# Optimization experiments

Measured on AMD Instinct MI355X. Metric: run time of the kernel, lower is better.

## Reference

```python
import jax, jax.numpy as jnp
import numpy as np

B, N_ELEC, N_NUC, D_EMB, D_MSG = 512, 32, 8, 128, 128


def idx_perm(n):
    # ordered pairs (i, j), i != j, shaped [n, n-1]
    i = np.repeat(np.arange(n), n - 1).reshape(n, n - 1)
    j = np.array([[k for k in range(n) if k != ii] for ii in range(n)])
    return jnp.asarray(i), jnp.asarray(j)


def pairwise_diffs(a, b):
    # a: [..., n, 3], b: [..., m, 3] -> [..., n, m, 4] (dx, dy, dz, |d|^2)
    d = a[..., :, None, :] - b[..., None, :, :]
    return jnp.concatenate([d, jnp.sum(d * d, axis=-1, keepdims=True)], axis=-1)


def mlp(x, w1, b1, w2, b2):
    return jax.nn.silu(x @ w1 + b1) @ w2 + b2


def setup_inputs() -> dict:
    key = jax.random.key(0)
    ks = jax.random.split(key, 10)
    sc = 0.1
    return {
        'rs': jax.random.normal(ks[0], (B, N_ELEC, 3), jnp.float32),
        'coords': jax.random.normal(ks[1], (N_NUC, 3), jnp.float32),
        'messages_el': jax.random.normal(ks[2], (B, N_ELEC, N_ELEC - 1, D_MSG), jnp.float32),
        'messages_nuc': jax.random.normal(ks[3], (B, N_ELEC, N_NUC, D_MSG), jnp.float32),
        'emb': jax.random.normal(ks[4], (B, N_ELEC, D_EMB), jnp.float32),
        'w1_el': jax.random.normal(ks[5], (D_EMB + D_MSG, 256), jnp.float32) * sc,
        'b1_el': jnp.zeros((256,), jnp.float32),
        'w2_el': jax.random.normal(ks[6], (256, 1), jnp.float32) * sc,
        'b2_el': jnp.zeros((1,), jnp.float32),
        'w1_nuc': jax.random.normal(ks[7], (D_EMB + D_MSG, 256), jnp.float32) * sc,
        'b1_nuc': jnp.zeros((256,), jnp.float32),
        'w2_nuc': jax.random.normal(ks[8], (256, 1), jnp.float32) * sc,
        'b2_nuc': jnp.zeros((1,), jnp.float32),
        'nuc_charges': jnp.array([6.0, 1.0, 1.0, 1.0, 1.0, 1.0, 1.0, 1.0], jnp.float32),
    }


def reference(rs, coords, messages_el, messages_nuc, emb,
              w1_el, b1_el, w2_el, b2_el,
              w1_nuc, b1_nuc, w2_nuc, b2_nuc, nuc_charges):
    n_elec, n_nuc = rs.shape[-2], coords.shape[0]
    emb_p = emb[:, :, None]  # [B, n_elec, 1, D_emb]
    # gather-concat features per pair
    f_el = jnp.concatenate(
        [jnp.broadcast_to(emb_p, (B, n_elec, n_elec - 1, D_EMB)), messages_el], axis=-1)
    f_nuc = jnp.concatenate(
        [jnp.broadcast_to(emb_p, (B, n_elec, n_nuc, D_EMB)), messages_nuc], axis=-1)
    i, j = idx_perm(n_elec)
    diffs_nuc = pairwise_diffs(rs, coords)  # [B, n_elec, n_nuc, 4]
    diffs_ee = pairwise_diffs(-rs, -rs)[:, i, j]  # [B, n_elec, n_elec-1, 4]
    diffs = jnp.concatenate([diffs_ee, diffs_nuc], axis=-2)
    f = jnp.concatenate(
        [mlp(f_el, w1_el, b1_el, w2_el, b2_el),
         mlp(f_nuc, w1_nuc, b1_nuc, w2_nuc, b2_nuc)], axis=-2)  # [B, n_elec, P, 1]
    ps = f * diffs[..., :3] / (1.0 + diffs[..., 3:] ** 1.5)
    ps = ps.sum(axis=-2)  # [B, n_elec, 3]
    # deeperwin decay
    decay = jnp.tanh(diffs_nuc[..., -1] / (0.5 / nuc_charges) ** 2).prod(axis=-1)
    return np.exp(-3.5).astype(np.float32) * decay[..., None] * ps
```

## Files before the change

kernel.cpp:

```cpp
#include <hip/hip_runtime.h>
#include <hip/hip_bf16.h>

#define OUT_SCALE 0.030197383422318501f

typedef __attribute__((ext_vector_type(8))) short bf16x8;
typedef __attribute__((ext_vector_type(4))) float f32x4;

#define EL_BLOCKS 2048
#define NUC_BLOCKS 1024

__device__ __forceinline__ unsigned pk2(float a, float b) {
  __hip_bfloat162 h = __float22bfloat162_rn(make_float2(a, b));
  unsigned u;
  __builtin_memcpy(&u, &h, 4);
  return u;
}

__device__ __forceinline__ float silu_f(float h) {
  return h * __builtin_amdgcn_rcpf(1.0f + __expf(-h));
}

__global__ void prep_w1(const float* __restrict__ w1a,
                        const float* __restrict__ w1b,
                        unsigned short* __restrict__ wp) {
  int gid = blockIdx.x * 256 + threadIdx.x;
  const float* w1 = (gid < 8192) ? w1a : w1b;
  int rem = gid & 8191;
  int kk = rem >> 10;
  int kg = (rem >> 8) & 3;
  int col = rem & 255;
  const float* src = w1 + (kk * 32 + kg * 8) * 256 + col;
  uint4 v;
  v.x = pk2(src[0 * 256], src[1 * 256]);
  v.y = pk2(src[2 * 256], src[3 * 256]);
  v.z = pk2(src[4 * 256], src[5 * 256]);
  v.w = pk2(src[6 * 256], src[7 * 256]);
  *(uint4*)(wp + (size_t)gid * 8) = v;
}

__global__ __launch_bounds__(512, 4) void bf_main_kernel(
    const float* __restrict__ rs, const float* __restrict__ msg_el,
    const float* __restrict__ msg_nuc, const float* __restrict__ emb,
    const unsigned short* __restrict__ wpk,
    const float* __restrict__ b1_el, const float* __restrict__ w2_el,
    const float* __restrict__ b2_el,
    const float* __restrict__ b1_nuc, const float* __restrict__ w2_nuc,
    const float* __restrict__ b2_nuc,
    const float* __restrict__ coords, const float* __restrict__ chg,
    float* __restrict__ out) {
  __shared__ __align__(16) unsigned short s_emb[16 * 128];
  __shared__ __align__(16) unsigned short s_msg[2 * 64 * 128];
  __shared__ __align__(16) float s_embc[16 * 256];
  __shared__ float s_fp[8][256];
  __shared__ float s_ps[16][4];
  __shared__ float s_decay[16];

  const int tid = threadIdx.x;
  const int bid = blockIdx.x;
  const int lane = tid & 63;
  const int wv = tid >> 6;
  const int cIdx = lane & 15, kg = lane >> 4;

  if (bid < EL_BLOCKS) {
    const int gp0 = bid * 8;
    const float* msg = msg_el;

    if (tid < 32) ((float*)s_ps)[tid] = 0.0f;

    {
      int p = tid >> 4, ch = tid & 15;
      if (tid < 128) {
        const float* src = emb + (gp0 + p) * 128 + ch * 8;
        float4 v0 = *(const float4*)src;
        float4 v1 = *(const float4*)(src + 4);
        uint4 pk;
        pk.x = pk2(v0.x, v0.y); pk.y = pk2(v0.z, v0.w);
        pk.z = pk2(v1.x, v1.y); pk.w = pk2(v1.z, v1.w);
        *(uint4*)(s_emb + p * 128 + (ch ^ (p & 15)) * 8) = pk;
      } else if (tid < 256) {
        uint4 z = {0u, 0u, 0u, 0u};
        *(uint4*)(s_emb + p * 128 + (ch ^ (p & 15)) * 8) = z;
      }
    }

    bf16x8 Bf[4][2];
    float b1v[2][4], w2v[2][4];
    const int col = wv * 32 + cIdx;
#pragma unroll
    for (int nt = 0; nt < 2; ++nt) {
#pragma unroll
      for (int reg = 0; reg < 4; ++reg) {
        int h = wv * 32 + nt * 16 + kg * 4 + reg;
        b1v[nt][reg] = b1_el[h];
        w2v[nt][reg] = w2_el[h];
      }
#pragma unroll
      for (int kk = 0; kk < 4; ++kk)
        Bf[kk][nt] = *(const bf16x8*)(
            wpk + (size_t)((kk * 4 + kg) * 256 + col + nt * 16) * 8);
    }

    float4 la[2], lb[2];
    bool lv[2];
#pragma unroll
    for (int u = 0; u < 2; ++u) {
      int id = u * 512 + tid;
      int lr = id >> 4, ch = id & 15;
      int p = lr >> 5, j = lr & 31;
      lv[u] = j < 31;
      const float* src =
          msg + (size_t)((gp0 + p) * 31 + (lv[u] ? j : 30)) * 128 + ch * 8;
      la[u] = *(const float4*)src;
      lb[u] = *(const float4*)(src + 4);
    }

    __syncthreads();

    {
      f32x4 aE0 = {b1v[0][0], b1v[0][1], b1v[0][2], b1v[0][3]};
      f32x4 aE1 = {b1v[1][0], b1v[1][1], b1v[1][2], b1v[1][3]};
#pragma unroll
      for (int kk = 0; kk < 4; ++kk) {
        bf16x8 a = *(const bf16x8*)(
            s_emb + cIdx * 128 + ((kk * 4 + kg) ^ (cIdx & 15)) * 8);
        aE0 = __builtin_amdgcn_mfma_f32_16x16x32_bf16(Bf[kk][0], a, aE0, 0, 0, 0);
        aE1 = __builtin_amdgcn_mfma_f32_16x16x32_bf16(Bf[kk][1], a, aE1, 0, 0, 0);
      }
      if (cIdx < 8) {
        *(f32x4*)(s_embc + cIdx * 256 + wv * 32 + kg * 4) = aE0;
        *(f32x4*)(s_embc + cIdx * 256 + wv * 32 + 16 + kg * 4) = aE1;
      }
    }

#pragma unroll
    for (int nt = 0; nt < 2; ++nt)
#pragma unroll
      for (int kk = 0; kk < 4; ++kk)
        Bf[kk][nt] = *(const bf16x8*)(
            wpk + (size_t)(((kk + 4) * 4 + kg) * 256 + col + nt * 16) * 8);

#pragma unroll
    for (int u = 0; u < 2; ++u) {
      int id = u * 512 + tid;
      int lr = id >> 4, ch = id & 15;
      uint4 pk;
      pk.x = lv[u] ? pk2(la[u].x, la[u].y) : 0u;
      pk.y = lv[u] ? pk2(la[u].z, la[u].w) : 0u;
      pk.z = lv[u] ? pk2(lb[u].x, lb[u].y) : 0u;
      pk.w = lv[u] ? pk2(lb[u].z, lb[u].w) : 0u;
      *(uint4*)(s_msg + lr * 128 + ((ch ^ (lr & 15)) * 8)) = pk;
    }

    __syncthreads();

#pragma unroll 1
    for (int c = 0; c < 4; ++c) {
      if (c < 3) {
#pragma unroll
        for (int u = 0; u < 2; ++u) {
          int id = u * 512 + tid;
          int lr = id >> 4, ch = id & 15;
          int row = (c + 1) * 64 + lr;
          int p = row >> 5, j = row & 31;
          lv[u] = j < 31;
          const float* src =
              msg + (size_t)((gp0 + p) * 31 + (lv[u] ? j : 30)) * 128 + ch * 8;
          la[u] = *(const float4*)src;
          lb[u] = *(const float4*)(src + 4);
        }
      }
      const unsigned short* mb = s_msg + (c & 1) * 8192;
#pragma unroll
      for (int tt = 0; tt < 4; ++tt) {
        int t = c * 4 + tt;
        int p = t >> 1;
        int r = t * 16 + cIdx;
        f32x4 acc0 = *(const f32x4*)(s_embc + p * 256 + wv * 32 + kg * 4);
        f32x4 acc1 = *(const f32x4*)(s_embc + p * 256 + wv * 32 + 16 + kg * 4);
        const unsigned short* mp = mb + (r & 63) * 128;
#pragma unroll
        for (int kk = 0; kk < 4; ++kk) {
          bf16x8 a = *(const bf16x8*)(mp + ((kk * 4 + kg) ^ (r & 15)) * 8);
          acc0 = __builtin_amdgcn_mfma_f32_16x16x32_bf16(Bf[kk][0], a, acc0, 0, 0, 0);
          acc1 = __builtin_amdgcn_mfma_f32_16x16x32_bf16(Bf[kk][1], a, acc1, 0, 0, 0);
        }
        float p0 = 0.0f, p1 = 0.0f;
#pragma unroll
        for (int reg = 0; reg < 4; ++reg) {
          p0 += silu_f(acc0[reg]) * w2v[0][reg];
          p1 += silu_f(acc1[reg]) * w2v[1][reg];
        }
        float v = p0 + p1;
        v += __shfl_xor(v, 16);
        v += __shfl_xor(v, 32);
        if (kg == 0) s_fp[wv][t * 16 + cIdx] = v;
      }
      if (c < 3) {
#pragma unroll
        for (int u = 0; u < 2; ++u) {
          int id = u * 512 + tid;
          int lr = id >> 4, ch = id & 15;
          uint4 pk;
          pk.x = lv[u] ? pk2(la[u].x, la[u].y) : 0u;
          pk.y = lv[u] ? pk2(la[u].z, la[u].w) : 0u;
          pk.z = lv[u] ? pk2(lb[u].x, lb[u].y) : 0u;
          pk.w = lv[u] ? pk2(lb[u].z, lb[u].w) : 0u;
          *(uint4*)(s_msg + ((c + 1) & 1) * 8192 + lr * 128 +
                    ((ch ^ (lr & 15)) * 8)) = pk;
        }
      }
      __syncthreads();
    }

    if (tid < 248) {
      int p = tid / 31, jj = tid - p * 31;
      int gp = gp0 + p, b = gp >> 5, i = gp & 31;
      int jidx = jj + (jj >= i ? 1 : 0);
      const float* rsb = rs + b * 96;
      float dx = rsb[jidx * 3 + 0] - rsb[i * 3 + 0];
      float dy = rsb[jidx * 3 + 1] - rsb[i * 3 + 1];
      float dz = rsb[jidx * 3 + 2] - rsb[i * 3 + 2];
      float tq = dx * dx + dy * dy + dz * dz;
      int row = p * 32 + jj;
      float f = b2_el[0];
#pragma unroll
      for (int w = 0; w < 8; ++w) f += s_fp[w][row];
      float g = f * __builtin_amdgcn_rcpf(1.0f + tq * sqrtf(tq));
      atomicAdd(&s_ps[p][0], g * dx);
      atomicAdd(&s_ps[p][1], g * dy);
      atomicAdd(&s_ps[p][2], g * dz);
    }
    if (tid < 8) {
      int gp = gp0 + tid, b = gp >> 5, i = gp & 31;
      float x = rs[(b * 32 + i) * 3 + 0];
      float y = rs[(b * 32 + i) * 3 + 1];
      float z = rs[(b * 32 + i) * 3 + 2];
      float dcy = 1.0f;
#pragma unroll
      for (int n = 0; n < 8; ++n) {
        float dx = x - coords[n * 3 + 0];
        float dy = y - coords[n * 3 + 1];
        float dz = z - coords[n * 3 + 2];
        float tq = dx * dx + dy * dy + dz * dz;
        float zc = chg[n];
        dcy *= tanhf(4.0f * tq * zc * zc);
      }
      s_decay[tid] = dcy;
    }
    __syncthreads();
    if (tid < 24) {
      int p = tid / 3, c = tid - p * 3;
      int gp = gp0 + p;
      atomicAdd(&out[gp * 3 + c], OUT_SCALE * s_decay[p] * s_ps[p][c]);
    }
  } else {
    const int nbid = bid - EL_BLOCKS;
    const int gp0 = nbid * 16;
    const float* msg = msg_nuc;
    const unsigned short* wp = wpk + 8192 * 8;

    if (tid < 64) ((float*)s_ps)[tid] = 0.0f;

    if (tid < 256) {
      int p = tid >> 4, ch = tid & 15;
      const float* src = emb + (gp0 + p) * 128 + ch * 8;
      float4 v0 = *(const float4*)src;
      float4 v1 = *(const float4*)(src + 4);
      uint4 pk;
      pk.x = pk2(v0.x, v0.y); pk.y = pk2(v0.z, v0.w);
      pk.z = pk2(v1.x, v1.y); pk.w = pk2(v1.z, v1.w);
      *(uint4*)(s_emb + p * 128 + (ch ^ (p & 15)) * 8) = pk;
    }

    bf16x8 Bf[4][2];
    float b1v[2][4], w2v[2][4];
    const int col = wv * 32 + cIdx;
#pragma unroll
    for (int nt = 0; nt < 2; ++nt) {
#pragma unroll
      for (int reg = 0; reg < 4; ++reg) {
        int h = wv * 32 + nt * 16 + kg * 4 + reg;
        b1v[nt][reg] = b1_nuc[h];
        w2v[nt][reg] = w2_nuc[h];
      }
#pragma unroll
      for (int kk = 0; kk < 4; ++kk)
        Bf[kk][nt] = *(const bf16x8*)(
            wp + (size_t)((kk * 4 + kg) * 256 + col + nt * 16) * 8);
    }

    float4 la[2], lb[2];
#pragma unroll
    for (int u = 0; u < 2; ++u) {
      int id = u * 512 + tid;
      int lr = id >> 4, ch = id & 15;
      const float* src = msg + (size_t)(gp0 * 8 + lr) * 128 + ch * 8;
      la[u] = *(const float4*)src;
      lb[u] = *(const float4*)(src + 4);
    }

    __syncthreads();

    {
      f32x4 aE0 = {b1v[0][0], b1v[0][1], b1v[0][2], b1v[0][3]};
      f32x4 aE1 = {b1v[1][0], b1v[1][1], b1v[1][2], b1v[1][3]};
#pragma unroll
      for (int kk = 0; kk < 4; ++kk) {
        bf16x8 a = *(const bf16x8*)(
            s_emb + cIdx * 128 + ((kk * 4 + kg) ^ (cIdx & 15)) * 8);
        aE0 = __builtin_amdgcn_mfma_f32_16x16x32_bf16(Bf[kk][0], a, aE0, 0, 0, 0);
        aE1 = __builtin_amdgcn_mfma_f32_16x16x32_bf16(Bf[kk][1], a, aE1, 0, 0, 0);
      }
      *(f32x4*)(s_embc + cIdx * 256 + wv * 32 + kg * 4) = aE0;
      *(f32x4*)(s_embc + cIdx * 256 + wv * 32 + 16 + kg * 4) = aE1;
    }

#pragma unroll
    for (int nt = 0; nt < 2; ++nt)
#pragma unroll
      for (int kk = 0; kk < 4; ++kk)
        Bf[kk][nt] = *(const bf16x8*)(
            wp + (size_t)(((kk + 4) * 4 + kg) * 256 + col + nt * 16) * 8);

#pragma unroll
    for (int u = 0; u < 2; ++u) {
      int id = u * 512 + tid;
      int lr = id >> 4, ch = id & 15;
      uint4 pk;
      pk.x = pk2(la[u].x, la[u].y);
      pk.y = pk2(la[u].z, la[u].w);
      pk.z = pk2(lb[u].x, lb[u].y);
      pk.w = pk2(lb[u].z, lb[u].w);
      *(uint4*)(s_msg + lr * 128 + ((ch ^ (lr & 15)) * 8)) = pk;
    }

    __syncthreads();

#pragma unroll 1
    for (int c = 0; c < 2; ++c) {
      if (c < 1) {
#pragma unroll
        for (int u = 0; u < 2; ++u) {
          int id = u * 512 + tid;
          int lr = id >> 4, ch = id & 15;
          const float* src =
              msg + (size_t)(gp0 * 8 + 64 + lr) * 128 + ch * 8;
          la[u] = *(const float4*)src;
          lb[u] = *(const float4*)(src + 4);
        }
      }
      const unsigned short* mb = s_msg + (c & 1) * 8192;
#pragma unroll
      for (int tt = 0; tt < 4; ++tt) {
        int t = c * 4 + tt;
        int r = t * 16 + cIdx;
        int p = r >> 3;
        f32x4 acc0 = *(const f32x4*)(s_embc + p * 256 + wv * 32 + kg * 4);
        f32x4 acc1 = *(const f32x4*)(s_embc + p * 256 + wv * 32 + 16 + kg * 4);
        const unsigned short* mp = mb + (r & 63) * 128;
#pragma unroll
        for (int kk = 0; kk < 4; ++kk) {
          bf16x8 a = *(const bf16x8*)(mp + ((kk * 4 + kg) ^ (r & 15)) * 8);
          acc0 = __builtin_amdgcn_mfma_f32_16x16x32_bf16(Bf[kk][0], a, acc0, 0, 0, 0);
          acc1 = __builtin_amdgcn_mfma_f32_16x16x32_bf16(Bf[kk][1], a, acc1, 0, 0, 0);
        }
        float p0 = 0.0f, p1 = 0.0f;
#pragma unroll
        for (int reg = 0; reg < 4; ++reg) {
          p0 += silu_f(acc0[reg]) * w2v[0][reg];
          p1 += silu_f(acc1[reg]) * w2v[1][reg];
        }
        float v = p0 + p1;
        v += __shfl_xor(v, 16);
        v += __shfl_xor(v, 32);
        if (kg == 0) s_fp[wv][t * 16 + cIdx] = v;
      }
      if (c < 1) {
#pragma unroll
        for (int u = 0; u < 2; ++u) {
          int id = u * 512 + tid;
          int lr = id >> 4, ch = id & 15;
          uint4 pk;
          pk.x = pk2(la[u].x, la[u].y);
          pk.y = pk2(la[u].z, la[u].w);
          pk.z = pk2(lb[u].x, lb[u].y);
          pk.w = pk2(lb[u].z, lb[u].w);
          *(uint4*)(s_msg + 8192 + lr * 128 + ((ch ^ (lr & 15)) * 8)) = pk;
        }
      }
      __syncthreads();
    }

    if (tid < 128) {
      int p = tid >> 3, n = tid & 7;
      int gp = gp0 + p, b = gp >> 5, i = gp & 31;
      float dx = rs[(b * 32 + i) * 3 + 0] - coords[n * 3 + 0];
      float dy = rs[(b * 32 + i) * 3 + 1] - coords[n * 3 + 1];
      float dz = rs[(b * 32 + i) * 3 + 2] - coords[n * 3 + 2];
      float tq = dx * dx + dy * dy + dz * dz;
      float f = b2_nuc[0];
#pragma unroll
      for (int w = 0; w < 8; ++w) f += s_fp[w][tid];
      float g = f * __builtin_amdgcn_rcpf(1.0f + tq * sqrtf(tq));
      atomicAdd(&s_ps[p][0], g * dx);
      atomicAdd(&s_ps[p][1], g * dy);
      atomicAdd(&s_ps[p][2], g * dz);
    }
    if (tid < 16) {
      int gp = gp0 + tid, b = gp >> 5, i = gp & 31;
      float x = rs[(b * 32 + i) * 3 + 0];
      float y = rs[(b * 32 + i) * 3 + 1];
      float z = rs[(b * 32 + i) * 3 + 2];
      float dcy = 1.0f;
#pragma unroll
      for (int n = 0; n < 8; ++n) {
        float dx = x - coords[n * 3 + 0];
        float dy = y - coords[n * 3 + 1];
        float dz = z - coords[n * 3 + 2];
        float tq = dx * dx + dy * dy + dz * dz;
        float zc = chg[n];
        dcy *= tanhf(4.0f * tq * zc * zc);
      }
      s_decay[tid] = dcy;
    }
    __syncthreads();
    if (tid < 48) {
      int p = tid / 3, c = tid - p * 3;
      int gp = gp0 + p;
      atomicAdd(&out[gp * 3 + c], OUT_SCALE * s_decay[p] * s_ps[p][c]);
    }
  }
}

extern "C" void kernel_launch(void* const* d_in, const int* in_sizes, int n_in,
                              void* d_out, int out_size, void* d_ws, size_t ws_size,
                              hipStream_t stream) {
  const float* rs       = (const float*)d_in[0];
  const float* coords   = (const float*)d_in[1];
  const float* msg_el   = (const float*)d_in[2];
  const float* msg_nuc  = (const float*)d_in[3];
  const float* emb      = (const float*)d_in[4];
  const float* w1_el    = (const float*)d_in[5];
  const float* b1_el    = (const float*)d_in[6];
  const float* w2_el    = (const float*)d_in[7];
  const float* b2_el    = (const float*)d_in[8];
  const float* w1_nuc   = (const float*)d_in[9];
  const float* b1_nuc   = (const float*)d_in[10];
  const float* w2_nuc   = (const float*)d_in[11];
  const float* b2_nuc   = (const float*)d_in[12];
  const float* chg      = (const float*)d_in[13];
  float* out = (float*)d_out;

  unsigned short* wpk = (unsigned short*)d_ws;

  hipMemsetAsync(out, 0, (size_t)out_size * sizeof(float), stream);
  prep_w1<<<64, 256, 0, stream>>>(w1_el, w1_nuc, wpk);
  bf_main_kernel<<<EL_BLOCKS + NUC_BLOCKS, 512, 0, stream>>>(
      rs, msg_el, msg_nuc, emb, wpk, b1_el, w2_el, b2_el, b1_nuc, w2_nuc,
      b2_nuc, coords, chg, out);
}
```

Measured before the change: 120.8 us.

## Process sixteen electrons per electron-pair block and drop padding zeroing

Electron-pair blocks now handle 16 electrons each instead of 8, halving the electron block count. The per-block embedding projection fills the full 16-row MFMA tile instead of zero-padding half of it, and the weight fragment loads are amortized over twice the work. Padded pair rows are loaded from a duplicate row rather than zeroed, since their outputs are unused. In exchange, each block does a longer serial chunk loop and uses more shared memory, and the grid has fewer blocks for latency hiding.

Result: faster. 114.8 us, median of 2 (-4.9%).

```diff
diff --git a/kernel.cpp b/kernel.cpp
--- a/kernel.cpp
+++ b/kernel.cpp
@@ -6,7 +6,7 @@
 typedef __attribute__((ext_vector_type(8))) short bf16x8;
 typedef __attribute__((ext_vector_type(4))) float f32x4;
 
-#define EL_BLOCKS 2048
+#define EL_BLOCKS 1024
 #define NUC_BLOCKS 1024
 
 __device__ __forceinline__ unsigned pk2(float a, float b) {
@@ -51,7 +51,7 @@
   __shared__ __align__(16) unsigned short s_emb[16 * 128];
   __shared__ __align__(16) unsigned short s_msg[2 * 64 * 128];
   __shared__ __align__(16) float s_embc[16 * 256];
-  __shared__ float s_fp[8][256];
+  __shared__ float s_fp[8][512];
   __shared__ float s_ps[16][4];
   __shared__ float s_decay[16];
 
@@ -62,25 +62,20 @@
   const int cIdx = lane & 15, kg = lane >> 4;
 
   if (bid < EL_BLOCKS) {
-    const int gp0 = bid * 8;
+    const int gp0 = bid * 16;
     const float* msg = msg_el;
 
-    if (tid < 32) ((float*)s_ps)[tid] = 0.0f;
-
-    {
+    if (tid < 64) ((float*)s_ps)[tid] = 0.0f;
+
+    if (tid < 256) {
       int p = tid >> 4, ch = tid & 15;
-      if (tid < 128) {
-        const float* src = emb + (gp0 + p) * 128 + ch * 8;
-        float4 v0 = *(const float4*)src;
-        float4 v1 = *(const float4*)(src + 4);
-        uint4 pk;
-        pk.x = pk2(v0.x, v0.y); pk.y = pk2(v0.z, v0.w);
-        pk.z = pk2(v1.x, v1.y); pk.w = pk2(v1.z, v1.w);
-        *(uint4*)(s_emb + p * 128 + (ch ^ (p & 15)) * 8) = pk;
-      } else if (tid < 256) {
-        uint4 z = {0u, 0u, 0u, 0u};
-        *(uint4*)(s_emb + p * 128 + (ch ^ (p & 15)) * 8) = z;
-      }
+      const float* src = emb + (gp0 + p) * 128 + ch * 8;
+      float4 v0 = *(const float4*)src;
+      float4 v1 = *(const float4*)(src + 4);
+      uint4 pk;
+      pk.x = pk2(v0.x, v0.y); pk.y = pk2(v0.z, v0.w);
+      pk.z = pk2(v1.x, v1.y); pk.w = pk2(v1.z, v1.w);
+      *(uint4*)(s_emb + p * 128 + (ch ^ p) * 8) = pk;
     }
 
     bf16x8 Bf[4][2];
@@ -101,17 +96,15 @@
     }
 
     float4 la[2], lb[2];
-    bool lv[2];
 #pragma unroll
     for (int u = 0; u < 2; ++u) {
       int id = u * 512 + tid;
-      int lr = id >> 4, ch = id & 15;
-      int p = lr >> 5, j = lr & 31;
-      lv[u] = j < 31;
-      const float* src =
-          msg + (size_t)((gp0 + p) * 31 + (lv[u] ? j : 30)) * 128 + ch * 8;
-      la[u] = *(const float4*)src;
-      lb[u] = *(const float4*)(src + 4);
+      int lrw = id >> 4, ch = id & 15;
+      int p = lrw >> 5, j = lrw & 31;
+      int jc = j < 31 ? j : 30;
+      const float* s = msg + (size_t)((gp0 + p) * 31 + jc) * 128 + ch * 8;
+      la[u] = *(const float4*)s;
+      lb[u] = *(const float4*)(s + 4);
     }
 
     __syncthreads();
@@ -122,14 +115,12 @@
 #pragma unroll
       for (int kk = 0; kk < 4; ++kk) {
         bf16x8 a = *(const bf16x8*)(
-            s_emb + cIdx * 128 + ((kk * 4 + kg) ^ (cIdx & 15)) * 8);
+            s_emb + cIdx * 128 + ((kk * 4 + kg) ^ cIdx) * 8);
         aE0 = __builtin_amdgcn_mfma_f32_16x16x32_bf16(Bf[kk][0], a, aE0, 0, 0, 0);
         aE1 = __builtin_amdgcn_mfma_f32_16x16x32_bf16(Bf[kk][1], a, aE1, 0, 0, 0);
       }
-      if (cIdx < 8) {
-        *(f32x4*)(s_embc + cIdx * 256 + wv * 32 + kg * 4) = aE0;
-        *(f32x4*)(s_embc + cIdx * 256 + wv * 32 + 16 + kg * 4) = aE1;
-      }
+      *(f32x4*)(s_embc + cIdx * 256 + wv * 32 + kg * 4) = aE0;
+      *(f32x4*)(s_embc + cIdx * 256 + wv * 32 + 16 + kg * 4) = aE1;
     }
 
 #pragma unroll
@@ -142,45 +133,41 @@
 #pragma unroll
     for (int u = 0; u < 2; ++u) {
       int id = u * 512 + tid;
-      int lr = id >> 4, ch = id & 15;
+      int lrw = id >> 4, ch = id & 15;
       uint4 pk;
-      pk.x = lv[u] ? pk2(la[u].x, la[u].y) : 0u;
-      pk.y = lv[u] ? pk2(la[u].z, la[u].w) : 0u;
-      pk.z = lv[u] ? pk2(lb[u].x, lb[u].y) : 0u;
-      pk.w = lv[u] ? pk2(lb[u].z, lb[u].w) : 0u;
-      *(uint4*)(s_msg + lr * 128 + ((ch ^ (lr & 15)) * 8)) = pk;
+      pk.x = pk2(la[u].x, la[u].y); pk.y = pk2(la[u].z, la[u].w);
+      pk.z = pk2(lb[u].x, lb[u].y); pk.w = pk2(lb[u].z, lb[u].w);
+      *(uint4*)(s_msg + lrw * 128 + ((ch ^ (lrw & 15)) * 8)) = pk;
     }
 
     __syncthreads();
 
 #pragma unroll 1
-    for (int c = 0; c < 4; ++c) {
-      if (c < 3) {
+    for (int c = 0; c < 8; ++c) {
+      if (c < 7) {
 #pragma unroll
         for (int u = 0; u < 2; ++u) {
           int id = u * 512 + tid;
-          int lr = id >> 4, ch = id & 15;
-          int row = (c + 1) * 64 + lr;
-          int p = row >> 5, j = row & 31;
-          lv[u] = j < 31;
-          const float* src =
-              msg + (size_t)((gp0 + p) * 31 + (lv[u] ? j : 30)) * 128 + ch * 8;
-          la[u] = *(const float4*)src;
-          lb[u] = *(const float4*)(src + 4);
+          int lrw = id >> 4, ch = id & 15;
+          int p = ((c + 1) << 1) + (lrw >> 5);
+          int j = lrw & 31;
+          int jc = j < 31 ? j : 30;
+          const float* s = msg + (size_t)((gp0 + p) * 31 + jc) * 128 + ch * 8;
+          la[u] = *(const float4*)s;
+          lb[u] = *(const float4*)(s + 4);
         }
       }
       const unsigned short* mb = s_msg + (c & 1) * 8192;
 #pragma unroll
       for (int tt = 0; tt < 4; ++tt) {
-        int t = c * 4 + tt;
-        int p = t >> 1;
-        int r = t * 16 + cIdx;
-        f32x4 acc0 = *(const f32x4*)(s_embc + p * 256 + wv * 32 + kg * 4);
-        f32x4 acc1 = *(const f32x4*)(s_embc + p * 256 + wv * 32 + 16 + kg * 4);
-        const unsigned short* mp = mb + (r & 63) * 128;
+        int p = (c << 1) + (tt >> 1);
+        const float* ec = s_embc + p * 256;
+        f32x4 acc0 = *(const f32x4*)(ec + wv * 32 + kg * 4);
+        f32x4 acc1 = *(const f32x4*)(ec + wv * 32 + 16 + kg * 4);
+        const unsigned short* mp = mb + (tt * 16 + cIdx) * 128;
 #pragma unroll
         for (int kk = 0; kk < 4; ++kk) {
-          bf16x8 a = *(const bf16x8*)(mp + ((kk * 4 + kg) ^ (r & 15)) * 8);
+          bf16x8 a = *(const bf16x8*)(mp + ((kk * 4 + kg) ^ cIdx) * 8);
           acc0 = __builtin_amdgcn_mfma_f32_16x16x32_bf16(Bf[kk][0], a, acc0, 0, 0, 0);
           acc1 = __builtin_amdgcn_mfma_f32_16x16x32_bf16(Bf[kk][1], a, acc1, 0, 0, 0);
         }
@@ -193,26 +180,24 @@
         float v = p0 + p1;
         v += __shfl_xor(v, 16);
         v += __shfl_xor(v, 32);
-        if (kg == 0) s_fp[wv][t * 16 + cIdx] = v;
-      }
-      if (c < 3) {
+        if (kg == 0) s_fp[wv][c * 64 + tt * 16 + cIdx] = v;
+      }
+      if (c < 7) {
 #pragma unroll
         for (int u = 0; u < 2; ++u) {
           int id = u * 512 + tid;
-          int lr = id >> 4, ch = id & 15;
+          int lrw = id >> 4, ch = id & 15;
           uint4 pk;
-          pk.x = lv[u] ? pk2(la[u].x, la[u].y) : 0u;
-          pk.y = lv[u] ? pk2(la[u].z, la[u].w) : 0u;
-          pk.z = lv[u] ? pk2(lb[u].x, lb[u].y) : 0u;
-          pk.w = lv[u] ? pk2(lb[u].z, lb[u].w) : 0u;
-          *(uint4*)(s_msg + ((c + 1) & 1) * 8192 + lr * 128 +
-                    ((ch ^ (lr & 15)) * 8)) = pk;
+          pk.x = pk2(la[u].x, la[u].y); pk.y = pk2(la[u].z, la[u].w);
+          pk.z = pk2(lb[u].x, lb[u].y); pk.w = pk2(lb[u].z, lb[u].w);
+          *(uint4*)(s_msg + ((c + 1) & 1) * 8192 + lrw * 128 +
+                    ((ch ^ (lrw & 15)) * 8)) = pk;
         }
       }
       __syncthreads();
     }
 
-    if (tid < 248) {
+    if (tid < 496) {
       int p = tid / 31, jj = tid - p * 31;
       int gp = gp0 + p, b = gp >> 5, i = gp & 31;
       int jidx = jj + (jj >= i ? 1 : 0);
@@ -230,7 +215,7 @@
       atomicAdd(&s_ps[p][1], g * dy);
       atomicAdd(&s_ps[p][2], g * dz);
     }
-    if (tid < 8) {
+    if (tid < 16) {
       int gp = gp0 + tid, b = gp >> 5, i = gp & 31;
       float x = rs[(b * 32 + i) * 3 + 0];
       float y = rs[(b * 32 + i) * 3 + 1];
@@ -248,7 +233,7 @@
       s_decay[tid] = dcy;
     }
     __syncthreads();
-    if (tid < 24) {
+    if (tid < 48) {
       int p = tid / 3, c = tid - p * 3;
       int gp = gp0 + p;
       atomicAdd(&out[gp * 3 + c], OUT_SCALE * s_decay[p] * s_ps[p][c]);
@@ -269,7 +254,7 @@
       uint4 pk;
       pk.x = pk2(v0.x, v0.y); pk.y = pk2(v0.z, v0.w);
       pk.z = pk2(v1.x, v1.y); pk.w = pk2(v1.z, v1.w);
-      *(uint4*)(s_emb + p * 128 + (ch ^ (p & 15)) * 8) = pk;
+      *(uint4*)(s_emb + p * 128 + (ch ^ p) * 8) = pk;
     }
 
     bf16x8 Bf[4][2];
@@ -293,10 +278,10 @@
 #pragma unroll
     for (int u = 0; u < 2; ++u) {
       int id = u * 512 + tid;
-      int lr = id >> 4, ch = id & 15;
-      const float* src = msg + (size_t)(gp0 * 8 + lr) * 128 + ch * 8;
-      la[u] = *(const float4*)src;
-      lb[u] = *(const float4*)(src + 4);
+      int lrw = id >> 4, ch = id & 15;
+      const float* s = msg + (size_t)(gp0 * 8 + lrw) * 128 + ch * 8;
+      la[u] = *(const float4*)s;
+      lb[u] = *(const float4*)(s + 4);
     }
 
     __syncthreads();
@@ -307,7 +292,7 @@
 #pragma unroll
       for (int kk = 0; kk < 4; ++kk) {
         bf16x8 a = *(const bf16x8*)(
-            s_emb + cIdx * 128 + ((kk * 4 + kg) ^ (cIdx & 15)) * 8);
+            s_emb + cIdx * 128 + ((kk * 4 + kg) ^ cIdx) * 8);
         aE0 = __builtin_amdgcn_mfma_f32_16x16x32_bf16(Bf[kk][0], a, aE0, 0, 0, 0);
         aE1 = __builtin_amdgcn_mfma_f32_16x16x32_bf16(Bf[kk][1], a, aE1, 0, 0, 0);
       }
@@ -325,13 +310,11 @@
 #pragma unroll
     for (int u = 0; u < 2; ++u) {
       int id = u * 512 + tid;
-      int lr = id >> 4, ch = id & 15;
+      int lrw = id >> 4, ch = id & 15;
       uint4 pk;
-      pk.x = pk2(la[u].x, la[u].y);
-      pk.y = pk2(la[u].z, la[u].w);
-      pk.z = pk2(lb[u].x, lb[u].y);
-      pk.w = pk2(lb[u].z, lb[u].w);
-      *(uint4*)(s_msg + lr * 128 + ((ch ^ (lr & 15)) * 8)) = pk;
+      pk.x = pk2(la[u].x, la[u].y); pk.y = pk2(la[u].z, la[u].w);
+      pk.z = pk2(lb[u].x, lb[u].y); pk.w = pk2(lb[u].z, lb[u].w);
+      *(uint4*)(s_msg + lrw * 128 + ((ch ^ (lrw & 15)) * 8)) = pk;
     }
 
     __syncthreads();
@@ -342,11 +325,10 @@
 #pragma unroll
         for (int u = 0; u < 2; ++u) {
           int id = u * 512 + tid;
-          int lr = id >> 4, ch = id & 15;
-          const float* src =
-              msg + (size_t)(gp0 * 8 + 64 + lr) * 128 + ch * 8;
-          la[u] = *(const float4*)src;
-          lb[u] = *(const float4*)(src + 4);
+          int lrw = id >> 4, ch = id & 15;
+          const float* s = msg + (size_t)(gp0 * 8 + 64 + lrw) * 128 + ch * 8;
+          la[u] = *(const float4*)s;
+          lb[u] = *(const float4*)(s + 4);
         }
       }
       const unsigned short* mb = s_msg + (c & 1) * 8192;
@@ -355,12 +337,13 @@
         int t = c * 4 + tt;
         int r = t * 16 + cIdx;
         int p = r >> 3;
-        f32x4 acc0 = *(const f32x4*)(s_embc + p * 256 + wv * 32 + kg * 4);
-        f32x4 acc1 = *(const f32x4*)(s_embc + p * 256 + wv * 32 + 16 + kg * 4);
+        const float* ec = s_embc + p * 256;
+        f32x4 acc0 = *(const f32x4*)(ec + wv * 32 + kg * 4);
+        f32x4 acc1 = *(const f32x4*)(ec + wv * 32 + 16 + kg * 4);
         const unsigned short* mp = mb + (r & 63) * 128;
 #pragma unroll
         for (int kk = 0; kk < 4; ++kk) {
-          bf16x8 a = *(const bf16x8*)(mp + ((kk * 4 + kg) ^ (r & 15)) * 8);
+          bf16x8 a = *(const bf16x8*)(mp + ((kk * 4 + kg) ^ cIdx) * 8);
           acc0 = __builtin_amdgcn_mfma_f32_16x16x32_bf16(Bf[kk][0], a, acc0, 0, 0, 0);
           acc1 = __builtin_amdgcn_mfma_f32_16x16x32_bf16(Bf[kk][1], a, acc1, 0, 0, 0);
         }
@@ -379,13 +362,11 @@
 #pragma unroll
         for (int u = 0; u < 2; ++u) {
           int id = u * 512 + tid;
-          int lr = id >> 4, ch = id & 15;
+          int lrw = id >> 4, ch = id & 15;
           uint4 pk;
-          pk.x = pk2(la[u].x, la[u].y);
-          pk.y = pk2(la[u].z, la[u].w);
-          pk.z = pk2(lb[u].x, lb[u].y);
-          pk.w = pk2(lb[u].z, lb[u].w);
-          *(uint4*)(s_msg + 8192 + lr * 128 + ((ch ^ (lr & 15)) * 8)) = pk;
+          pk.x = pk2(la[u].x, la[u].y); pk.y = pk2(la[u].z, la[u].w);
+          pk.z = pk2(lb[u].x, lb[u].y); pk.w = pk2(lb[u].z, lb[u].w);
+          *(uint4*)(s_msg + 8192 + lrw * 128 + ((ch ^ (lrw & 15)) * 8)) = pk;
         }
       }
       __syncthreads();
```
